# Kernel optimization log

Measured on AMD Instinct MI355X. Metric: run time of the kernel, lower is better.

## Reference

```python
import jax, jax.numpy as jnp
import numpy as np

N = 8192
F_IN = 256
F_OUT = 64
ALPHA = 0.2  # LeakyReLU negative slope
EDGE_P = 0.004  # ~33 avg degree


def setup_inputs() -> dict:
    key = jax.random.key(0)
    k1, k2, k3, k4 = jax.random.split(key, 4)
    h = jax.random.normal(k1, (N, F_IN), dtype=jnp.float32)
    # xavier-ish scale for params
    W = jax.random.normal(k2, (F_IN, F_OUT), dtype=jnp.float32) * np.float32(np.sqrt(2.0 / (F_IN + F_OUT)))
    a = jax.random.normal(k3, (2 * F_OUT, 1), dtype=jnp.float32) * np.float32(np.sqrt(2.0 / (2 * F_OUT + 1)))
    adj = (jax.random.uniform(k4, (N, N)) < EDGE_P).astype(jnp.float32)
    return {"h": h, "adj": adj, "W": W, "a": a}


def reference(h, adj, W, a):
    f_out = W.shape[1]
    Wh = h @ W  # [N, F_OUT]
    # NOTE: original uses a[out_features:] for the source (row) term
    wh1 = Wh @ a[f_out:, :]  # [N, 1]
    wh2 = Wh @ a[:f_out, :]  # [N, 1]
    # e[u, i] = wh1[u] + wh2[i] only where adj nonzero; zero elsewhere (NO -inf mask,
    # faithful to the original: softmax sees zeros at non-edges)
    e = jnp.where(adj != 0, wh1 + wh2.T, jnp.float32(0.0))  # [N, N]
    e = jnp.where(e >= 0, e, ALPHA * e)  # LeakyReLU
    attention = jax.nn.softmax(e, axis=1)  # [N, N]
    # dropout p=0.0 -> identity
    h_prime = attention @ Wh  # [N, F_OUT]
    return jax.nn.elu(h_prime)  # concat=True
```

## Files before the change

### kernel.cpp

```cpp
#include <hip/hip_runtime.h>
#include <hip/hip_bf16.h>
#include <math.h>

#define N     8192
#define F_IN  256
#define F_OUT 64
#define ALPHA 0.2f

__global__ __launch_bounds__(256) void gat_wh_kernel(
    const float* __restrict__ h,
    const float* __restrict__ W,
    const float* __restrict__ a,
    float* __restrict__ Wh,
    float* __restrict__ wh1,
    float* __restrict__ wh2,
    float* __restrict__ colpart)
{
    __shared__ float s_h[32][F_IN];
    __shared__ float s_cp[256];

    const int tid = threadIdx.x;
    const int wv  = tid >> 6;
    const int ln  = tid & 63;
    const int rowbase = blockIdx.x * 32;

    const float4* hsrc = (const float4*)(h + (size_t)rowbase * F_IN);
    float4* hdst = (float4*)&s_h[0][0];
#pragma unroll
    for (int i = 0; i < 8; ++i) hdst[tid + 256 * i] = hsrc[tid + 256 * i];
    __syncthreads();

    const int r0 = wv * 8;
    float acc[8] = {0.f, 0.f, 0.f, 0.f, 0.f, 0.f, 0.f, 0.f};

#pragma unroll 4
    for (int k2 = 0; k2 < F_IN / 2; ++k2) {
        const int k = k2 * 2;
        const float wk0 = W[(k + 0) * F_OUT + ln];
        const float wk1 = W[(k + 1) * F_OUT + ln];
#pragma unroll
        for (int r = 0; r < 8; ++r) {
            const float2 hv = *(const float2*)&s_h[r0 + r][k];
            acc[r] += hv.x * wk0 + hv.y * wk1;
        }
    }

    const float a2 = a[ln];
    const float a1 = a[F_OUT + ln];
    float colacc = 0.f;

#pragma unroll
    for (int r = 0; r < 8; ++r) {
        const int u = rowbase + r0 + r;
        Wh[(size_t)u * F_OUT + ln] = acc[r];
        colacc += acc[r];
        float p1 = acc[r] * a1;
        float p2 = acc[r] * a2;
#pragma unroll
        for (int off = 32; off > 0; off >>= 1) {
            p1 += __shfl_down(p1, off);
            p2 += __shfl_down(p2, off);
        }
        if (ln == 0) { wh1[u] = p1; wh2[u] = p2; }
    }

    s_cp[tid] = colacc;
    __syncthreads();
    if (tid < 64) {
        colpart[(size_t)blockIdx.x * 64 + tid] =
            s_cp[tid] + s_cp[tid + 64] + s_cp[tid + 128] + s_cp[tid + 192];
    }
}

__global__ __launch_bounds__(256) void gat_colsum_kernel(
    const float* __restrict__ colpart,
    float* __restrict__ colsum)
{
    __shared__ float r[256];
    const int tid = threadIdx.x;
    const int f = tid & 63;
    const int g = tid >> 6;
    float s = 0.f;
    for (int b = g; b < 256; b += 4) s += colpart[(size_t)b * 64 + f];
    r[tid] = s;
    __syncthreads();
    if (tid < 64) {
        colsum[f] = r[f] + r[f + 64] + r[f + 128] + r[f + 192];
    }
}

__global__ __launch_bounds__(256) void gat_main_kernel(
    const float* __restrict__ adj,
    const float* __restrict__ Wh,
    const float* __restrict__ wh1,
    const float* __restrict__ wh2,
    const float* __restrict__ colsum,
    float* __restrict__ out)
{
    const int tid  = threadIdx.x;
    const int lane = tid & 63;
    const int wv   = tid >> 6;
    const int u    = blockIdx.x * 4 + wv;

    const float wh1u = wh1[u];
    const float* __restrict__ arow = adj + (size_t)u * N;

    float acc  = 0.f;
    float sumw = 0.f;

    const float4* p0 = (const float4*)arow + lane * 4;
    float4 b0 = p0[0], b1 = p0[1], b2 = p0[2], b3 = p0[3];

    for (int it = 0; it < 8; ++it) {
        const float4 v0 = b0, v1 = b1, v2 = b2, v3 = b3;
        if (it < 7) {
            const float4* np = (const float4*)(arow + (it + 1) * 1024) + lane * 4;
            b0 = np[0]; b1 = np[1]; b2 = np[2]; b3 = np[3];
        }
        const int cbase = it * 1024;
        const float vals[16] = {v0.x, v0.y, v0.z, v0.w, v1.x, v1.y, v1.z, v1.w,
                                v2.x, v2.y, v2.z, v2.w, v3.x, v3.y, v3.z, v3.w};
#pragma unroll
        for (int j = 0; j < 16; ++j) {
            const bool nz = (vals[j] != 0.f);
            float w_own = 0.f;
            if (nz) {
                float e = wh1u + wh2[cbase + lane * 16 + j];
                e = (e >= 0.f) ? e : ALPHA * e;
                w_own = expm1f(e);
            }
            unsigned long long m = __ballot(nz);
            while (m) {
                const int l = __ffsll((long long)m) - 1;
                m &= m - 1;
                const float w = __shfl(w_own, l);
                const int col = cbase + (l << 4) + j;
                sumw += w;
                acc += w * Wh[((size_t)col << 6) + lane];
            }
        }
    }

    const float val = (acc + colsum[lane]) / (sumw + (float)N);
    out[((size_t)u << 6) + lane] = (val > 0.f) ? val : expm1f(val);
}

extern "C" void kernel_launch(void* const* d_in, const int* in_sizes, int n_in,
                              void* d_out, int out_size, void* d_ws, size_t ws_size,
                              hipStream_t stream) {
    const float* h   = (const float*)d_in[0];
    const float* adj = (const float*)d_in[1];
    const float* W   = (const float*)d_in[2];
    const float* a   = (const float*)d_in[3];
    float* out = (float*)d_out;

    float* ws      = (float*)d_ws;
    float* Wh      = ws;
    float* wh1     = Wh + (size_t)N * F_OUT;
    float* wh2     = wh1 + N;
    float* colpart = wh2 + N;
    float* colsum  = colpart + 256 * 64;

    gat_wh_kernel<<<N / 32, 256, 0, stream>>>(h, W, a, Wh, wh1, wh2, colpart);
    gat_colsum_kernel<<<1, 256, 0, stream>>>(colpart, colsum);
    gat_main_kernel<<<N / 4, 256, 0, stream>>>(adj, Wh, wh1, wh2, colsum, out);
}
```

Measured before the change: 415.8 us.

## Split dense adjacency scan into edge-list build plus compact gather kernel

Result: slower. 459.3 us (+10.5%).

```diff
diff --git a/kernel.cpp b/kernel.cpp
--- a/kernel.cpp
+++ b/kernel.cpp
@@ -6,6 +6,7 @@
 #define F_IN  256
 #define F_OUT 64
 #define ALPHA 0.2f
+#define MAXE  192
 
 __global__ __launch_bounds__(256) void gat_wh_kernel(
     const float* __restrict__ h,
@@ -14,24 +15,30 @@
     float* __restrict__ Wh,
     float* __restrict__ wh1,
     float* __restrict__ wh2,
-    float* __restrict__ colpart)
+    float* __restrict__ colpart,
+    int*   __restrict__ cnt)
 {
-    __shared__ float s_h[32][F_IN];
+    __shared__ float s_h[16][F_IN];
     __shared__ float s_cp[256];
 
     const int tid = threadIdx.x;
     const int wv  = tid >> 6;
     const int ln  = tid & 63;
-    const int rowbase = blockIdx.x * 32;
+    const int rowbase = blockIdx.x * 16;
 
-    const float4* hsrc = (const float4*)(h + (size_t)rowbase * F_IN);
-    float4* hdst = (float4*)&s_h[0][0];
+    const int gtid = blockIdx.x * 256 + tid;
+    if (gtid < N) cnt[gtid] = 0;
+
+    {
+        const float4* hsrc = (const float4*)(h + (size_t)rowbase * F_IN);
+        float4* hdst = (float4*)&s_h[0][0];
 #pragma unroll
-    for (int i = 0; i < 8; ++i) hdst[tid + 256 * i] = hsrc[tid + 256 * i];
+        for (int i = 0; i < 4; ++i) hdst[tid + 256 * i] = hsrc[tid + 256 * i];
+    }
     __syncthreads();
 
-    const int r0 = wv * 8;
-    float acc[8] = {0.f, 0.f, 0.f, 0.f, 0.f, 0.f, 0.f, 0.f};
+    const int r0 = wv * 4;
+    float acc[4] = {0.f, 0.f, 0.f, 0.f};
 
 #pragma unroll 4
     for (int k2 = 0; k2 < F_IN / 2; ++k2) {
@@ -39,7 +46,7 @@
         const float wk0 = W[(k + 0) * F_OUT + ln];
         const float wk1 = W[(k + 1) * F_OUT + ln];
 #pragma unroll
-        for (int r = 0; r < 8; ++r) {
+        for (int r = 0; r < 4; ++r) {
             const float2 hv = *(const float2*)&s_h[r0 + r][k];
             acc[r] += hv.x * wk0 + hv.y * wk1;
         }
@@ -48,9 +55,8 @@
     const float a2 = a[ln];
     const float a1 = a[F_OUT + ln];
     float colacc = 0.f;
-
 #pragma unroll
-    for (int r = 0; r < 8; ++r) {
+    for (int r = 0; r < 4; ++r) {
         const int u = rowbase + r0 + r;
         Wh[(size_t)u * F_OUT + ln] = acc[r];
         colacc += acc[r];
@@ -81,68 +87,82 @@
     const int f = tid & 63;
     const int g = tid >> 6;
     float s = 0.f;
-    for (int b = g; b < 256; b += 4) s += colpart[(size_t)b * 64 + f];
+    for (int b = g; b < 512; b += 4) s += colpart[(size_t)b * 64 + f];
     r[tid] = s;
     __syncthreads();
-    if (tid < 64) {
-        colsum[f] = r[f] + r[f + 64] + r[f + 128] + r[f + 192];
+    if (tid < 64) colsum[f] = r[f] + r[f + 64] + r[f + 128] + r[f + 192];
+}
+
+__global__ __launch_bounds__(256) void gat_edge_kernel(
+    const float* __restrict__ adj,
+    int* __restrict__ cnt,
+    int* __restrict__ cols)
+{
+    const int tid = threadIdx.x;
+    const int ln  = tid & 63;
+    const int wv  = tid >> 6;
+    const int u   = blockIdx.x * 4 + wv;
+
+    const float* __restrict__ arow = adj + (size_t)u * N;
+    int* __restrict__ rowcols = cols + (size_t)u * MAXE;
+
+#pragma unroll 2
+    for (int it = 0; it < 16; ++it) {
+        const int base = it * 512 + ln * 8;
+        const float4 v0 = *(const float4*)(arow + base);
+        const float4 v1 = *(const float4*)(arow + base + 4);
+        const float vals[8] = {v0.x, v0.y, v0.z, v0.w, v1.x, v1.y, v1.z, v1.w};
+#pragma unroll
+        for (int j = 0; j < 8; ++j) {
+            if (vals[j] != 0.f) {
+                const int pos = atomicAdd(&cnt[u], 1);
+                if (pos < MAXE) rowcols[pos] = base + j;
+            }
+        }
     }
 }
 
-__global__ __launch_bounds__(256) void gat_main_kernel(
-    const float* __restrict__ adj,
+__global__ __launch_bounds__(256) void gat_gather_kernel(
+    const int*   __restrict__ cnt,
+    const int*   __restrict__ cols,
     const float* __restrict__ Wh,
     const float* __restrict__ wh1,
     const float* __restrict__ wh2,
     const float* __restrict__ colsum,
     float* __restrict__ out)
 {
-    const int tid  = threadIdx.x;
-    const int lane = tid & 63;
-    const int wv   = tid >> 6;
-    const int u    = blockIdx.x * 4 + wv;
+    const int tid = threadIdx.x;
+    const int ln  = tid & 63;
+    const int wv  = tid >> 6;
+    const int u   = blockIdx.x * 4 + wv;
 
+    const int n = min(cnt[u], MAXE);
     const float wh1u = wh1[u];
-    const float* __restrict__ arow = adj + (size_t)u * N;
+    const int* __restrict__ rowcols = cols + (size_t)u * MAXE;
 
     float acc  = 0.f;
     float sumw = 0.f;
 
-    const float4* p0 = (const float4*)arow + lane * 4;
-    float4 b0 = p0[0], b1 = p0[1], b2 = p0[2], b3 = p0[3];
-
-    for (int it = 0; it < 8; ++it) {
-        const float4 v0 = b0, v1 = b1, v2 = b2, v3 = b3;
-        if (it < 7) {
-            const float4* np = (const float4*)(arow + (it + 1) * 1024) + lane * 4;
-            b0 = np[0]; b1 = np[1]; b2 = np[2]; b3 = np[3];
+    for (int b0 = 0; b0 < n; b0 += 64) {
+        const int m = min(64, n - b0);
+        int   col_own = 0;
+        float w_own   = 0.f;
+        if (ln < m) {
+            col_own = rowcols[b0 + ln];
+            float e = wh1u + wh2[col_own];
+            e = (e >= 0.f) ? e : ALPHA * e;
+            w_own = expm1f(e);
         }
-        const int cbase = it * 1024;
-        const float vals[16] = {v0.x, v0.y, v0.z, v0.w, v1.x, v1.y, v1.z, v1.w,
-                                v2.x, v2.y, v2.z, v2.w, v3.x, v3.y, v3.z, v3.w};
-#pragma unroll
-        for (int j = 0; j < 16; ++j) {
-            const bool nz = (vals[j] != 0.f);
-            float w_own = 0.f;
-            if (nz) {
-                float e = wh1u + wh2[cbase + lane * 16 + j];
-                e = (e >= 0.f) ? e : ALPHA * e;
-                w_own = expm1f(e);
-            }
-            unsigned long long m = __ballot(nz);
-            while (m) {
-                const int l = __ffsll((long long)m) - 1;
-                m &= m - 1;
-                const float w = __shfl(w_own, l);
-                const int col = cbase + (l << 4) + j;
-                sumw += w;
-                acc += w * Wh[((size_t)col << 6) + lane];
-            }
+        for (int l = 0; l < m; ++l) {
+            const int   col = __shfl(col_own, l);
+            const float w   = __shfl(w_own, l);
+            sumw += w;
+            acc += w * Wh[((size_t)col << 6) + ln];
         }
     }
 
-    const float val = (acc + colsum[lane]) / (sumw + (float)N);
-    out[((size_t)u << 6) + lane] = (val > 0.f) ? val : expm1f(val);
+    const float val = (acc + colsum[ln]) / (sumw + (float)N);
+    out[((size_t)u << 6) + ln] = (val > 0.f) ? val : expm1f(val);
 }
 
 extern "C" void kernel_launch(void* const* d_in, const int* in_sizes, int n_in,
@@ -159,9 +179,12 @@
     float* wh1     = Wh + (size_t)N * F_OUT;
     float* wh2     = wh1 + N;
     float* colpart = wh2 + N;
-    float* colsum  = colpart + 256 * 64;
+    float* colsum  = colpart + 512 * 64;
+    int*   cnt     = (int*)(colsum + 64);
+    int*   cols    = cnt + N;
 
-    gat_wh_kernel<<<N / 32, 256, 0, stream>>>(h, W, a, Wh, wh1, wh2, colpart);
+    gat_wh_kernel<<<N / 16, 256, 0, stream>>>(h, W, a, Wh, wh1, wh2, colpart, cnt);
+    gat_edge_kernel<<<N / 4, 256, 0, stream>>>(adj, cnt, cols);
     gat_colsum_kernel<<<1, 256, 0, stream>>>(colpart, colsum);
-    gat_main_kernel<<<N / 4, 256, 0, stream>>>(adj, Wh, wh1, wh2, colsum, out);
+    gat_gather_kernel<<<N / 4, 256, 0, stream>>>(cnt, cols, Wh, wh1, wh2, colsum, out);
 }
```
